# Optimization experiments

Measured on AMD Instinct MI355X. Metric: run time of the kernel, lower is better.

Reference implementation:

```python
import jax, jax.numpy as jnp
import numpy as np

B, H, W, C = 16, 64, 64, 256
DIM = 256

def setup_inputs() -> dict:
    key = jax.random.key(0)
    ks = jax.random.split(key, 9)
    s_in = 1.0 / np.sqrt(C)
    x = jax.random.normal(ks[0], (B, H, W, C), dtype=jnp.float32)
    Wq = jax.random.normal(ks[1], (C, DIM), dtype=jnp.float32) * s_in
    bq = jnp.zeros((DIM,), dtype=jnp.float32)
    Wk = jax.random.normal(ks[2], (C, DIM), dtype=jnp.float32) * s_in
    bk = jnp.zeros((DIM,), dtype=jnp.float32)
    Wv = jax.random.normal(ks[3], (C, DIM), dtype=jnp.float32) * s_in
    bv = jnp.zeros((DIM,), dtype=jnp.float32)
    # 'out' conv sees 1 input channel (after the channel reduce_sum)
    Wo = jax.random.normal(ks[4], (1, DIM), dtype=jnp.float32)
    bo = jnp.zeros((DIM,), dtype=jnp.float32)
    return {"x": x, "Wq": Wq, "bq": bq, "Wk": Wk, "bk": bk,
            "Wv": Wv, "bv": bv, "Wo": Wo, "bo": bo}

def reference(x, Wq, bq, Wk, bk, Wv, bv, Wo, bo):
    # 1x1 convs == channel GEMMs
    q = jnp.einsum('bhwc,cd->bhwd', x, Wq) + bq
    k = jnp.einsum('bhwc,cd->bhwd', x, Wk) + bk
    v = jnp.einsum('bhwc,cd->bhwd', x, Wv) + bv
    # channel-reduce score -> [B,H,W,1], softmax jointly over spatial axes
    score = jnp.sum(q * k, axis=-1, keepdims=True)
    attn = jax.nn.softmax(score, axis=(1, 2))
    # channel-reduce of v weighted by per-pixel attn -> [B,H,W,1]
    out = jnp.sum(v * attn, axis=-1, keepdims=True)
    # final 1x1 conv: 1 input channel -> DIM output channels
    return jnp.einsum('bhwc,cd->bhwd', out, Wo) + bo
```

## Files before the change

### kernel.cpp

```cpp
#include <hip/hip_runtime.h>


typedef __bf16 bf16_t;
typedef __attribute__((ext_vector_type(8))) __bf16 bf16x8;
typedef __attribute__((ext_vector_type(4))) float f32x4;

#define NBATCH 16
#define NPIX   65536
#define PPB    4096

#define MH_OFF    0u
#define ML_OFF    131072u
#define U_OFF     262144u
#define WV_OFF    263168u
#define SCL_OFF   264192u
#define SCORE_OFF 264448u
#define SV_OFF    526592u
#define BMAX_OFF  788736u
#define BSUM_OFF  788800u

__global__ __launch_bounds__(256) void prep_kernel(
    const float* __restrict__ Wq, const float* __restrict__ bq,
    const float* __restrict__ Wk, const float* __restrict__ bk,
    const float* __restrict__ Wv, const float* __restrict__ bv,
    bf16_t* __restrict__ Mh, bf16_t* __restrict__ Ml,
    float* __restrict__ u, float* __restrict__ wv, float* __restrict__ scl)
{
    const int t = threadIdx.x;
    if (blockIdx.x < 256) {
        const int c = blockIdx.x;
        __shared__ __align__(16) float wq_row[256];
        __shared__ __align__(16) float wk_row[256];
        wq_row[t] = Wq[c * 256 + t];
        wk_row[t] = Wk[c * 256 + t];
        __syncthreads();
        const float4* wkt = (const float4*)(Wk + t * 256);
        const float4* wqt = (const float4*)(Wq + t * 256);
        const float4* wq4 = (const float4*)wq_row;
        const float4* wk4 = (const float4*)wk_row;
        float d1 = 0.f, d2 = 0.f;
#pragma unroll 8
        for (int i = 0; i < 64; ++i) {
            float4 a = wq4[i], b = wkt[i];
            d1 += a.x * b.x + a.y * b.y + a.z * b.z + a.w * b.w;
            float4 e = wk4[i], f = wqt[i];
            d2 += e.x * f.x + e.y * f.y + e.z * f.z + e.w * f.w;
        }
        float m = 0.5f * (d1 + d2);
        bf16_t h = (bf16_t)m;
        bf16_t l = (bf16_t)(m - (float)h);
        Mh[c * 256 + t] = h;
        Ml[c * 256 + t] = l;
    } else {
        float uacc = 0.f, wvacc = 0.f;
        const float* wqr = Wq + t * 256;
        const float* wkr = Wk + t * 256;
        const float* wvr = Wv + t * 256;
#pragma unroll 4
        for (int d = 0; d < 256; ++d) {
            uacc += wqr[d] * bk[d] + wkr[d] * bq[d];
            wvacc += wvr[d];
        }
        u[t] = uacc;
        wv[t] = wvacc;
        __shared__ float r1[256], r2[256];
        r1[t] = bq[t] * bk[t];
        r2[t] = bv[t];
        __syncthreads();
        for (int s = 128; s > 0; s >>= 1) {
            if (t < s) { r1[t] += r1[t + s]; r2[t] += r2[t + s]; }
            __syncthreads();
        }
        if (t == 0) { scl[0] = r1[0]; scl[1] = r2[0]; }
    }
}

__device__ __forceinline__ int swz(int row, int col) {
    return row * 256 + (col ^ ((row & 7) << 3));
}

__device__ __forceinline__ float rowsum16(float v) {
    v += __int_as_float(__builtin_amdgcn_update_dpp(0, __float_as_int(v), 0x118, 0xF, 0xF, true));
    v += __int_as_float(__builtin_amdgcn_update_dpp(0, __float_as_int(v), 0x114, 0xF, 0xF, true));
    v += __int_as_float(__builtin_amdgcn_update_dpp(0, __float_as_int(v), 0x112, 0xF, 0xF, true));
    v += __int_as_float(__builtin_amdgcn_update_dpp(0, __float_as_int(v), 0x111, 0xF, 0xF, true));
    return v;
}

__global__ __launch_bounds__(512, 2) void score_kernel(
    const float* __restrict__ x,
    const bf16_t* __restrict__ Mh, const bf16_t* __restrict__ Ml,
    const float* __restrict__ u, const float* __restrict__ wvp,
    const float* __restrict__ scl,
    float* __restrict__ score, float* __restrict__ svout)
{
    __shared__ __align__(16) bf16_t Ah[64 * 256];
    __shared__ float redS[8][64];
    __shared__ float svp[64], tpp[64];

    const int t = threadIdx.x;
    const int lane = t & 63;
    const int wid = t >> 6;
    const int l15 = lane & 15;
    const int lg = lane >> 4;
    const int pix0 = blockIdx.x * 64;
    const int wcol0 = wid * 32;

    const int srow = t >> 3;
    const int sch = (t & 7) * 32;
    const float* xrow = x + (size_t)(pix0 + srow) * 256 + sch;

    float4 xv[8];
#pragma unroll
    for (int i = 0; i < 8; ++i) xv[i] = *(const float4*)(xrow + i * 4);
#pragma unroll
    for (int j = 0; j < 4; ++j) {
        bf16x8 hi;
#pragma unroll
        for (int e = 0; e < 8; ++e) hi[e] = (bf16_t)(((const float*)xv)[j * 8 + e]);
        *(bf16x8*)&Ah[swz(srow, sch + j * 8)] = hi;
    }
    float sv_acc = 0.f, tp_acc = 0.f;
#pragma unroll
    for (int i = 0; i < 8; ++i) {
        float4 wvv = *(const float4*)(wvp + sch + i * 4);
        float4 uvv = *(const float4*)(u + sch + i * 4);
        sv_acc += xv[i].x * wvv.x + xv[i].y * wvv.y + xv[i].z * wvv.z + xv[i].w * wvv.w;
        tp_acc += xv[i].x * uvv.x + xv[i].y * uvv.y + xv[i].z * uvv.z + xv[i].w * uvv.w;
    }
#pragma unroll
    for (int m = 1; m < 8; m <<= 1) {
        sv_acc += __shfl_xor(sv_acc, m, 64);
        tp_acc += __shfl_xor(tp_acc, m, 64);
    }
    if ((t & 7) == 0) { svp[srow] = sv_acc; tpp[srow] = tp_acc; }

    f32x4 acc[4][2];
#pragma unroll
    for (int i = 0; i < 4; ++i)
#pragma unroll
        for (int j = 0; j < 2; ++j)
            acc[i][j] = (f32x4){0.f, 0.f, 0.f, 0.f};

    __syncthreads();

    const int bbase = (wcol0 + l15) * 256 + lg * 8;
#pragma unroll
    for (int ks = 0; ks < 8; ++ks) {
        const int k0 = ks * 32;
        bf16x8 af[4];
#pragma unroll
        for (int rf = 0; rf < 4; ++rf)
            af[rf] = *(const bf16x8*)&Ah[swz(rf * 16 + l15, k0 + lg * 8)];
        bf16x8 bh[2], bl[2];
#pragma unroll
        for (int cf = 0; cf < 2; ++cf) {
            bh[cf] = *(const bf16x8*)(Mh + bbase + cf * 4096 + k0);
            bl[cf] = *(const bf16x8*)(Ml + bbase + cf * 4096 + k0);
        }
#pragma unroll
        for (int rf = 0; rf < 4; ++rf)
#pragma unroll
            for (int cf = 0; cf < 2; ++cf) {
                acc[rf][cf] = __builtin_amdgcn_mfma_f32_16x16x32_bf16(
                    af[rf], bh[cf], acc[rf][cf], 0, 0, 0);
                acc[rf][cf] = __builtin_amdgcn_mfma_f32_16x16x32_bf16(
                    af[rf], bl[cf], acc[rf][cf], 0, 0, 0);
            }
    }

#pragma unroll
    for (int rf = 0; rf < 4; ++rf) {
#pragma unroll
        for (int r = 0; r < 4; ++r) {
            int row = rf * 16 + lg * 4 + r;
            const float* xr = x + (size_t)(pix0 + row) * 256 + wcol0 + l15;
            float s = 0.f;
#pragma unroll
            for (int cf = 0; cf < 2; ++cf) {
                float xf = xr[cf * 16];
                float e2 = 2.f * xf - (float)(bf16_t)xf;
                s += e2 * acc[rf][cf][r];
            }
            s = rowsum16(s);
            if (l15 == 15) redS[wid][row] = s;
        }
    }
    __syncthreads();
    if (t < 64) {
        float s = tpp[t] + scl[0];
#pragma unroll
        for (int w = 0; w < 8; ++w) s += redS[w][t];
        score[pix0 + t] = s;
        svout[pix0 + t] = svp[t] + scl[1];
    }
}

__global__ __launch_bounds__(256) void stats_kernel(
    const float* __restrict__ score,
    float* __restrict__ bmax, float* __restrict__ bsum)
{
    const int b = blockIdx.x, t = threadIdx.x;
    const int lane = t & 63, wid = t >> 6;
    const float4* s4 = (const float4*)(score + b * PPB);
    float4 v[4];
#pragma unroll
    for (int i = 0; i < 4; ++i) v[i] = s4[t + i * 256];
    float m = v[0].x;
#pragma unroll
    for (int i = 0; i < 4; ++i) {
        m = fmaxf(m, fmaxf(fmaxf(v[i].x, v[i].y), fmaxf(v[i].z, v[i].w)));
    }
    float sum = 0.f;
#pragma unroll
    for (int i = 0; i < 4; ++i) {
        sum += __expf(v[i].x - m) + __expf(v[i].y - m) +
               __expf(v[i].z - m) + __expf(v[i].w - m);
    }
#pragma unroll
    for (int k = 1; k < 64; k <<= 1) {
        float om = __shfl_xor(m, k, 64);
        float os = __shfl_xor(sum, k, 64);
        float nm = fmaxf(m, om);
        sum = sum * __expf(m - nm) + os * __expf(om - nm);
        m = nm;
    }
    __shared__ float sm[4], ss[4];
    if (lane == 0) { sm[wid] = m; ss[wid] = sum; }
    __syncthreads();
    if (t == 0) {
        float M = fmaxf(fmaxf(sm[0], sm[1]), fmaxf(sm[2], sm[3]));
        float S = ss[0] * __expf(sm[0] - M) + ss[1] * __expf(sm[1] - M) +
                  ss[2] * __expf(sm[2] - M) + ss[3] * __expf(sm[3] - M);
        bmax[b] = M; bsum[b] = S;
    }
}

__global__ __launch_bounds__(256) void out_kernel(
    const float* __restrict__ score, const float* __restrict__ sv,
    const float* __restrict__ bmax, const float* __restrict__ bsum,
    const float* __restrict__ Wo, const float* __restrict__ bo,
    float* __restrict__ out)
{
    const int total = NPIX * 64;
    const int stride = gridDim.x * blockDim.x;
    for (int idx = blockIdx.x * blockDim.x + threadIdx.x; idx < total; idx += stride) {
        int p = idx >> 6;
        int c4 = (idx & 63) << 2;
        int b = p >> 12;
        float g = __expf(score[p] - bmax[b]) / bsum[b] * sv[p];
        float4 w = *(const float4*)(Wo + c4);
        float4 bb = *(const float4*)(bo + c4);
        float4 o = { g * w.x + bb.x, g * w.y + bb.y, g * w.z + bb.z, g * w.w + bb.w };
        *(float4*)(out + (size_t)p * 256 + c4) = o;
    }
}

extern "C" void kernel_launch(void* const* d_in, const int* in_sizes, int n_in,
                              void* d_out, int out_size, void* d_ws, size_t ws_size,
                              hipStream_t stream) {
    const float* x  = (const float*)d_in[0];
    const float* Wq = (const float*)d_in[1];
    const float* bq = (const float*)d_in[2];
    const float* Wk = (const float*)d_in[3];
    const float* bk = (const float*)d_in[4];
    const float* Wv = (const float*)d_in[5];
    const float* bv = (const float*)d_in[6];
    const float* Wo = (const float*)d_in[7];
    const float* bo = (const float*)d_in[8];
    float* out = (float*)d_out;
    char* ws = (char*)d_ws;

    bf16_t* Mh = (bf16_t*)(ws + MH_OFF);
    bf16_t* Ml = (bf16_t*)(ws + ML_OFF);
    float* u   = (float*)(ws + U_OFF);
    float* wv  = (float*)(ws + WV_OFF);
    float* scl = (float*)(ws + SCL_OFF);
    float* score = (float*)(ws + SCORE_OFF);
    float* sv    = (float*)(ws + SV_OFF);
    float* bmax  = (float*)(ws + BMAX_OFF);
    float* bsum  = (float*)(ws + BSUM_OFF);

    prep_kernel<<<dim3(257), dim3(256), 0, stream>>>(Wq, bq, Wk, bk, Wv, bv, Mh, Ml, u, wv, scl);
    score_kernel<<<dim3(NPIX / 64), dim3(512), 0, stream>>>(x, Mh, Ml, u, wv, scl, score, sv);
    stats_kernel<<<dim3(NBATCH), dim3(256), 0, stream>>>(score, bmax, bsum);
    out_kernel<<<dim3(4096), dim3(256), 0, stream>>>(score, sv, bmax, bsum, Wo, bo, out);
}
```

Baseline: 124.9 us.

## Load A fragments directly from global, drop LDS staging, widen per-wave column tile

Removes the shared-memory bf16 staging of the x tile and instead has each wave load fp32 x directly from global memory into MFMA A fragments, converting to bf16 in registers. Block size drops from 512 to 256 threads, with each wave covering 64 columns instead of 32, and the sv/tp dot products move into the epilogue using per-column reductions. This eliminates the LDS write, the barrier, and the swizzle at the cost of redundant global reads of x across the four waves, more accumulator registers, and lower occupancy (launch bounds 256,1).

```diff
diff --git a/kernel.cpp b/kernel.cpp
--- a/kernel.cpp
+++ b/kernel.cpp
@@ -75,10 +75,6 @@
     }
 }
 
-__device__ __forceinline__ int swz(int row, int col) {
-    return row * 256 + (col ^ ((row & 7) << 3));
-}
-
 __device__ __forceinline__ float rowsum16(float v) {
     v += __int_as_float(__builtin_amdgcn_update_dpp(0, __float_as_int(v), 0x118, 0xF, 0xF, true));
     v += __int_as_float(__builtin_amdgcn_update_dpp(0, __float_as_int(v), 0x114, 0xF, 0xF, true));
@@ -87,16 +83,21 @@
     return v;
 }
 
-__global__ __launch_bounds__(512, 2) void score_kernel(
+__device__ __forceinline__ bf16x8 cvt8(float4 a0, float4 a1) {
+    bf16x8 r;
+    r[0] = (bf16_t)a0.x; r[1] = (bf16_t)a0.y; r[2] = (bf16_t)a0.z; r[3] = (bf16_t)a0.w;
+    r[4] = (bf16_t)a1.x; r[5] = (bf16_t)a1.y; r[6] = (bf16_t)a1.z; r[7] = (bf16_t)a1.w;
+    return r;
+}
+
+__global__ __launch_bounds__(256, 1) void score_kernel(
     const float* __restrict__ x,
     const bf16_t* __restrict__ Mh, const bf16_t* __restrict__ Ml,
     const float* __restrict__ u, const float* __restrict__ wvp,
     const float* __restrict__ scl,
     float* __restrict__ score, float* __restrict__ svout)
 {
-    __shared__ __align__(16) bf16_t Ah[64 * 256];
-    __shared__ float redS[8][64];
-    __shared__ float svp[64], tpp[64];
+    __shared__ float redS[4][64], redV[4][64], redT[4][64];
 
     const int t = threadIdx.x;
     const int lane = t & 63;
@@ -104,64 +105,39 @@
     const int l15 = lane & 15;
     const int lg = lane >> 4;
     const int pix0 = blockIdx.x * 64;
-    const int wcol0 = wid * 32;
-
-    const int srow = t >> 3;
-    const int sch = (t & 7) * 32;
-    const float* xrow = x + (size_t)(pix0 + srow) * 256 + sch;
-
-    float4 xv[8];
-#pragma unroll
-    for (int i = 0; i < 8; ++i) xv[i] = *(const float4*)(xrow + i * 4);
-#pragma unroll
-    for (int j = 0; j < 4; ++j) {
-        bf16x8 hi;
-#pragma unroll
-        for (int e = 0; e < 8; ++e) hi[e] = (bf16_t)(((const float*)xv)[j * 8 + e]);
-        *(bf16x8*)&Ah[swz(srow, sch + j * 8)] = hi;
-    }
-    float sv_acc = 0.f, tp_acc = 0.f;
-#pragma unroll
-    for (int i = 0; i < 8; ++i) {
-        float4 wvv = *(const float4*)(wvp + sch + i * 4);
-        float4 uvv = *(const float4*)(u + sch + i * 4);
-        sv_acc += xv[i].x * wvv.x + xv[i].y * wvv.y + xv[i].z * wvv.z + xv[i].w * wvv.w;
-        tp_acc += xv[i].x * uvv.x + xv[i].y * uvv.y + xv[i].z * uvv.z + xv[i].w * uvv.w;
-    }
-#pragma unroll
-    for (int m = 1; m < 8; m <<= 1) {
-        sv_acc += __shfl_xor(sv_acc, m, 64);
-        tp_acc += __shfl_xor(tp_acc, m, 64);
-    }
-    if ((t & 7) == 0) { svp[srow] = sv_acc; tpp[srow] = tp_acc; }
-
-    f32x4 acc[4][2];
+    const int wcol0 = wid * 64;
+
+    f32x4 acc[4][4];
 #pragma unroll
     for (int i = 0; i < 4; ++i)
 #pragma unroll
-        for (int j = 0; j < 2; ++j)
+        for (int j = 0; j < 4; ++j)
             acc[i][j] = (f32x4){0.f, 0.f, 0.f, 0.f};
 
-    __syncthreads();
-
+    const float* xbase = x + (size_t)pix0 * 256;
     const int bbase = (wcol0 + l15) * 256 + lg * 8;
+
 #pragma unroll
     for (int ks = 0; ks < 8; ++ks) {
         const int k0 = ks * 32;
         bf16x8 af[4];
 #pragma unroll
-        for (int rf = 0; rf < 4; ++rf)
-            af[rf] = *(const bf16x8*)&Ah[swz(rf * 16 + l15, k0 + lg * 8)];
-        bf16x8 bh[2], bl[2];
-#pragma unroll
-        for (int cf = 0; cf < 2; ++cf) {
+        for (int rf = 0; rf < 4; ++rf) {
+            const float* ap = xbase + (rf * 16 + l15) * 256 + k0 + lg * 8;
+            float4 a0 = *(const float4*)ap;
+            float4 a1 = *(const float4*)(ap + 4);
+            af[rf] = cvt8(a0, a1);
+        }
+        bf16x8 bh[4], bl[4];
+#pragma unroll
+        for (int cf = 0; cf < 4; ++cf) {
             bh[cf] = *(const bf16x8*)(Mh + bbase + cf * 4096 + k0);
             bl[cf] = *(const bf16x8*)(Ml + bbase + cf * 4096 + k0);
         }
 #pragma unroll
         for (int rf = 0; rf < 4; ++rf)
 #pragma unroll
-            for (int cf = 0; cf < 2; ++cf) {
+            for (int cf = 0; cf < 4; ++cf) {
                 acc[rf][cf] = __builtin_amdgcn_mfma_f32_16x16x32_bf16(
                     af[rf], bh[cf], acc[rf][cf], 0, 0, 0);
                 acc[rf][cf] = __builtin_amdgcn_mfma_f32_16x16x32_bf16(
@@ -169,30 +145,48 @@
             }
     }
 
+    float wvc[4], uc[4];
+#pragma unroll
+    for (int cf = 0; cf < 4; ++cf) {
+        wvc[cf] = wvp[wcol0 + cf * 16 + l15];
+        uc[cf] = u[wcol0 + cf * 16 + l15];
+    }
 #pragma unroll
     for (int rf = 0; rf < 4; ++rf) {
 #pragma unroll
         for (int r = 0; r < 4; ++r) {
             int row = rf * 16 + lg * 4 + r;
-            const float* xr = x + (size_t)(pix0 + row) * 256 + wcol0 + l15;
-            float s = 0.f;
-#pragma unroll
-            for (int cf = 0; cf < 2; ++cf) {
+            const float* xr = xbase + (size_t)row * 256 + wcol0 + l15;
+            float s = 0.f, v = 0.f, tp = 0.f;
+#pragma unroll
+            for (int cf = 0; cf < 4; ++cf) {
                 float xf = xr[cf * 16];
                 float e2 = 2.f * xf - (float)(bf16_t)xf;
                 s += e2 * acc[rf][cf][r];
+                v += xf * wvc[cf];
+                tp += xf * uc[cf];
             }
             s = rowsum16(s);
-            if (l15 == 15) redS[wid][row] = s;
+            v = rowsum16(v);
+            tp = rowsum16(tp);
+            if (l15 == 15) {
+                redS[wid][row] = s;
+                redV[wid][row] = v;
+                redT[wid][row] = tp;
+            }
         }
     }
     __syncthreads();
     if (t < 64) {
-        float s = tpp[t] + scl[0];
-#pragma unroll
-        for (int w = 0; w < 8; ++w) s += redS[w][t];
+        float s = scl[0];
+        float v = scl[1];
+#pragma unroll
+        for (int w = 0; w < 4; ++w) {
+            s += redS[w][t] + redT[w][t];
+            v += redV[w][t];
+        }
         score[pix0 + t] = s;
-        svout[pix0 + t] = svp[t] + scl[1];
+        svout[pix0 + t] = v;
     }
 }
 
@@ -282,7 +276,7 @@
     float* bsum  = (float*)(ws + BSUM_OFF);
 
     prep_kernel<<<dim3(257), dim3(256), 0, stream>>>(Wq, bq, Wk, bk, Wv, bv, Mh, Ml, u, wv, scl);
-    score_kernel<<<dim3(NPIX / 64), dim3(512), 0, stream>>>(x, Mh, Ml, u, wv, scl, score, sv);
+    score_kernel<<<dim3(NPIX / 64), dim3(256), 0, stream>>>(x, Mh, Ml, u, wv, scl, score, sv);
     stats_kernel<<<dim3(NBATCH), dim3(256), 0, stream>>>(score, bmax, bsum);
     out_kernel<<<dim3(4096), dim3(256), 0, stream>>>(score, sv, bmax, bsum, Wo, bo, out);
 }
```

Result: slower. 132.4 us (+6.0%).
